# Optimization experiments

Measured on AMD Instinct MI355X. Metric: run time of the kernel, lower is better.

Reference implementation:

```python
import jax, jax.numpy as jnp
import numpy as np

N, E, H, DE = 50000, 800000, 128, 16

def silu(x):
    return x * jax.nn.sigmoid(x)

def setup_inputs() -> dict:
    key = jax.random.key(0)
    ks = jax.random.split(key, 24)
    def W(k, i, o, s=0.02):
        return (jax.random.normal(k, (i, o), jnp.float32) * s)
    inp = {
        'h': jax.random.normal(ks[0], (N, H), jnp.float32),
        'coord': jax.random.normal(ks[1], (N, 3), jnp.float32),
        'edge_index': jax.random.randint(ks[2], (2, E), 0, N),
        'edge_attr': jax.random.normal(ks[3], (E, DE), jnp.float32),
        # mes_mlp: Linear(2H+1+DE -> H), SiLU, Linear(H -> H), SiLU
        'mes_w1': W(ks[4], 2 * H + 1 + DE, H), 'mes_b1': jnp.zeros((H,), jnp.float32),
        'mes_w2': W(ks[5], H, H),              'mes_b2': jnp.zeros((H,), jnp.float32),
        # edge_mlp: Linear(H+1+DE -> H), SiLU, Linear(H -> H)
        'edge_w1': W(ks[6], H + 1 + DE, H),    'edge_b1': jnp.zeros((H,), jnp.float32),
        'edge_w2': W(ks[7], H, H),             'edge_b2': jnp.zeros((H,), jnp.float32),
        # node_mlp: Linear(H+H -> H), SiLU, Linear(H -> H)
        'node_w1': W(ks[8], 2 * H, H),         'node_b1': jnp.zeros((H,), jnp.float32),
        'node_w2': W(ks[9], H, H),             'node_b2': jnp.zeros((H,), jnp.float32),
        # coord_mlp: Linear(H -> H), SiLU, Linear(H -> 1, no bias, xavier gain 0.001)
        'coord_w1': W(ks[10], H, H),           'coord_b1': jnp.zeros((H,), jnp.float32),
        'coord_w2': W(ks[11], H, 1, s=0.001),
    }
    return inp

def reference(h, coord, edge_index, edge_attr,
              mes_w1, mes_b1, mes_w2, mes_b2,
              edge_w1, edge_b1, edge_w2, edge_b2,
              node_w1, node_b1, node_w2, node_b2,
              coord_w1, coord_b1, coord_w2):
    row, col = edge_index[0], edge_index[1]
    n = h.shape[0]
    # coord2radial
    coord_diff = coord[row] - coord[col]                        # [E,3]
    radial = jnp.sum(coord_diff ** 2, axis=1, keepdims=True)    # [E,1]
    norm = jnp.sqrt(radial + 1e-8)
    coord_diff = coord_diff / (norm + 1.0)
    # mes_model
    mes_in = jnp.concatenate([h[row], h[col], radial, edge_attr], axis=1)
    edge_feat = silu(silu(mes_in @ mes_w1 + mes_b1) @ mes_w2 + mes_b2)  # [E,H]
    # coord_model (agg='sum', no tanh)
    trans = coord_diff * (silu(edge_feat @ coord_w1 + coord_b1) @ coord_w2)  # [E,3]
    coord = coord + jax.ops.segment_sum(trans, col, num_segments=n)
    # node_model (recurrent)
    agg = jax.ops.segment_sum(edge_feat, col, num_segments=n)   # [N,H]
    node_in = jnp.concatenate([h, agg], axis=1)
    h = h + (silu(node_in @ node_w1 + node_b1) @ node_w2 + node_b2)
    # edge_model
    edge_in = jnp.concatenate([edge_feat, radial, edge_attr], axis=1)
    edge_out = silu(edge_in @ edge_w1 + edge_b1) @ edge_w2 + edge_b2
    return (h, coord, edge_out)
```

## Files before the change

kernel.cpp:

```cpp
#include <hip/hip_runtime.h>
#include <cstdint>
#include <cstddef>

typedef float f32x4 __attribute__((ext_vector_type(4)));
typedef __bf16 bf16x8 __attribute__((ext_vector_type(8)));
typedef unsigned short u16;

#define Hdim 128
#define DEdim 16
#define APITCH 296
#define FPITCH 168
#define NPITCH 264

__device__ __forceinline__ u16 f2bf(float f){
  uint32_t u = __builtin_bit_cast(uint32_t, f);
  u += 0x7fffu + ((u >> 16) & 1u);
  return (u16)(u >> 16);
}
__device__ __forceinline__ float silu_f(float x){
  return x / (1.0f + __expf(-x));
}

template<int KC>
__device__ __forceinline__ void gemm_tile(
    const u16* A, int apitch,
    const u16* __restrict__ Bt, int kpad,
    const float* __restrict__ bias,
    int wv, int cidx, int hi, f32x4 (&acc)[4][2])
{
  const int c0 = (wv*2+0)*16 + cidx;
  const int c1 = (wv*2+1)*16 + cidx;
  const float b0 = bias[c0];
  const float b1 = bias[c1];
  #pragma unroll
  for (int rt=0; rt<4; ++rt){
    acc[rt][0] = (f32x4){b0,b0,b0,b0};
    acc[rt][1] = (f32x4){b1,b1,b1,b1};
  }
  #pragma unroll
  for (int kc=0; kc<KC; ++kc){
    const int ko = kc*32 + hi*8;
    bf16x8 bb0 = *(const bf16x8*)(Bt + (size_t)c0*kpad + ko);
    bf16x8 bb1 = *(const bf16x8*)(Bt + (size_t)c1*kpad + ko);
    #pragma unroll
    for (int rt=0; rt<4; ++rt){
      bf16x8 a = *(const bf16x8*)(A + (rt*16+cidx)*apitch + ko);
      acc[rt][0] = __builtin_amdgcn_mfma_f32_16x16x32_bf16(a, bb0, acc[rt][0], 0,0,0);
      acc[rt][1] = __builtin_amdgcn_mfma_f32_16x16x32_bf16(a, bb1, acc[rt][1], 0,0,0);
    }
  }
}

__global__ __launch_bounds__(256, 2) void egcl_edge(
    const float* __restrict__ h, const float* __restrict__ coord,
    const int* __restrict__ ei, const float* __restrict__ ea,
    const float* __restrict__ mes_b1, const float* __restrict__ mes_b2,
    const float* __restrict__ edge_b1, const float* __restrict__ edge_b2,
    const float* __restrict__ coord_b1, const float* __restrict__ coord_w2,
    const u16* __restrict__ w_mes1t, const u16* __restrict__ w_mes2t,
    const u16* __restrict__ w_coord1t, const u16* __restrict__ w_edge1t,
    const u16* __restrict__ w_edge2t,
    float* __restrict__ agg, float* __restrict__ out_coord,
    float* __restrict__ out_edge, int E, int N)
{
  __shared__ u16 Ab[64*APITCH];
  __shared__ u16 Fb[64*FPITCH];
  __shared__ float cds[64*4];
  __shared__ float tvs[64];
  __shared__ int cnode[64];

  const int tid  = threadIdx.x;
  const int lane = tid & 63;
  const int wv   = tid >> 6;
  const int e0   = blockIdx.x * 64;
  const int cidx = lane & 15;
  const int hi   = lane >> 4;

  {
    const int le   = wv*16 + (lane>>2);
    const int part = lane & 3;
    int eg = e0 + le;
    if (eg >= E) eg = E-1;
    const int node = (part < 2) ? ei[eg] : ei[E + eg];
    const float* src = h + (size_t)node*Hdim + (part&1)*64;
    u16* dst = Ab + le*APITCH + part*64;
    #pragma unroll
    for (int j=0;j<16;++j){
      const float4 v = ((const float4*)src)[j];
      ushort4 o; o.x=f2bf(v.x); o.y=f2bf(v.y); o.z=f2bf(v.z); o.w=f2bf(v.w);
      *(ushort4*)(dst + j*4) = o;
    }
    if (part == 0){
      const int cn = ei[E + eg];
      const float dx = coord[(size_t)node*3+0] - coord[(size_t)cn*3+0];
      const float dy = coord[(size_t)node*3+1] - coord[(size_t)cn*3+1];
      const float dz = coord[(size_t)node*3+2] - coord[(size_t)cn*3+2];
      const float radial = dx*dx + dy*dy + dz*dz;
      const float inv = 1.0f/(sqrtf(radial + 1e-8f) + 1.0f);
      cds[le*4+0]=dx*inv; cds[le*4+1]=dy*inv; cds[le*4+2]=dz*inv; cds[le*4+3]=radial;
      cnode[le] = cn;
      const u16 rb = f2bf(radial);
      Ab[le*APITCH + 256] = rb;
      Fb[le*FPITCH + 128] = rb;
      #pragma unroll
      for (int j=0;j<DEdim;++j){
        const u16 v = f2bf(ea[(size_t)eg*DEdim + j]);
        Ab[le*APITCH + 257 + j] = v;
        Fb[le*FPITCH + 129 + j] = v;
      }
      #pragma unroll
      for (int j=273;j<288;++j) Ab[le*APITCH + j] = 0;
      #pragma unroll
      for (int j=145;j<160;++j) Fb[le*FPITCH + j] = 0;
    }
    if (tid < 64) tvs[tid] = 0.f;
  }
  __syncthreads();

  f32x4 acc[4][2];

  gemm_tile<9>(Ab, APITCH, w_mes1t, 288, mes_b1, wv, cidx, hi, acc);
  __syncthreads();
  #pragma unroll
  for (int rt=0; rt<4; ++rt)
    #pragma unroll
    for (int j=0;j<2;++j){
      const int col = (wv*2+j)*16 + cidx;
      #pragma unroll
      for (int i=0;i<4;++i)
        Ab[(rt*16 + hi*4 + i)*APITCH + col] = f2bf(silu_f(acc[rt][j][i]));
    }
  __syncthreads();

  gemm_tile<4>(Ab, APITCH, w_mes2t, 128, mes_b2, wv, cidx, hi, acc);
  #pragma unroll
  for (int rt=0; rt<4; ++rt)
    #pragma unroll
    for (int j=0;j<2;++j){
      const int col = (wv*2+j)*16 + cidx;
      #pragma unroll
      for (int i=0;i<4;++i){
        const int row = rt*16 + hi*4 + i;
        const float v = silu_f(acc[rt][j][i]);
        if (e0 + row < E)
          atomicAdd(agg + (size_t)cnode[row]*Hdim + col, v);
        Fb[row*FPITCH + col] = f2bf(v);
      }
    }
  __syncthreads();

  gemm_tile<4>(Fb, FPITCH, w_coord1t, 128, coord_b1, wv, cidx, hi, acc);
  {
    const float cw0 = coord_w2[(wv*2+0)*16 + cidx];
    const float cw1 = coord_w2[(wv*2+1)*16 + cidx];
    #pragma unroll
    for (int rt=0; rt<4; ++rt)
      #pragma unroll
      for (int i=0;i<4;++i){
        float p = silu_f(acc[rt][0][i])*cw0 + silu_f(acc[rt][1][i])*cw1;
        p += __shfl_xor(p, 1);
        p += __shfl_xor(p, 2);
        p += __shfl_xor(p, 4);
        p += __shfl_xor(p, 8);
        if (cidx == 0) atomicAdd(&tvs[rt*16 + hi*4 + i], p);
      }
  }
  __syncthreads();
  if (tid < 192){
    const int le = tid/3, d = tid%3;
    if (e0 + le < E)
      atomicAdd(out_coord + (size_t)cnode[le]*3 + d, cds[le*4+d]*tvs[le]);
  }

  gemm_tile<5>(Fb, FPITCH, w_edge1t, 160, edge_b1, wv, cidx, hi, acc);
  #pragma unroll
  for (int rt=0; rt<4; ++rt)
    #pragma unroll
    for (int j=0;j<2;++j){
      const int col = (wv*2+j)*16 + cidx;
      #pragma unroll
      for (int i=0;i<4;++i)
        Ab[(rt*16 + hi*4 + i)*APITCH + col] = f2bf(silu_f(acc[rt][j][i]));
    }
  __syncthreads();

  gemm_tile<4>(Ab, APITCH, w_edge2t, 128, edge_b2, wv, cidx, hi, acc);
  #pragma unroll
  for (int rt=0; rt<4; ++rt)
    #pragma unroll
    for (int j=0;j<2;++j){
      const int col = (wv*2+j)*16 + cidx;
      #pragma unroll
      for (int i=0;i<4;++i){
        const int row = rt*16 + hi*4 + i;
        const int eg = e0 + row;
        if (eg < E) out_edge[(size_t)eg*Hdim + col] = acc[rt][j][i];
      }
    }
}

__global__ __launch_bounds__(256, 2) void egcl_node(
    const float* __restrict__ h, const float* __restrict__ agg,
    const float* __restrict__ node_b1, const float* __restrict__ node_b2,
    const u16* __restrict__ w_node1t, const u16* __restrict__ w_node2t,
    float* __restrict__ out_h, int N)
{
  __shared__ u16 Ab[64*NPITCH];
  const int tid  = threadIdx.x;
  const int lane = tid & 63;
  const int wv   = tid >> 6;
  const int r0   = blockIdx.x * 64;
  const int cidx = lane & 15;
  const int hi   = lane >> 4;

  {
    const int le   = wv*16 + (lane>>2);
    const int part = lane & 3;
    int g = r0 + le;
    if (g >= N) g = N-1;
    const float* src = (part < 2) ? h   + (size_t)g*Hdim + part*64
                                  : agg + (size_t)g*Hdim + (part-2)*64;
    u16* dst = Ab + le*NPITCH + part*64;
    #pragma unroll
    for (int j=0;j<16;++j){
      const float4 v = ((const float4*)src)[j];
      ushort4 o; o.x=f2bf(v.x); o.y=f2bf(v.y); o.z=f2bf(v.z); o.w=f2bf(v.w);
      *(ushort4*)(dst + j*4) = o;
    }
  }
  __syncthreads();

  f32x4 acc[4][2];
  gemm_tile<8>(Ab, NPITCH, w_node1t, 256, node_b1, wv, cidx, hi, acc);
  __syncthreads();
  #pragma unroll
  for (int rt=0; rt<4; ++rt)
    #pragma unroll
    for (int j=0;j<2;++j){
      const int col = (wv*2+j)*16 + cidx;
      #pragma unroll
      for (int i=0;i<4;++i)
        Ab[(rt*16 + hi*4 + i)*NPITCH + col] = f2bf(silu_f(acc[rt][j][i]));
    }
  __syncthreads();
  gemm_tile<4>(Ab, NPITCH, w_node2t, 128, node_b2, wv, cidx, hi, acc);
  #pragma unroll
  for (int rt=0; rt<4; ++rt)
    #pragma unroll
    for (int j=0;j<2;++j){
      const int col = (wv*2+j)*16 + cidx;
      #pragma unroll
      for (int i=0;i<4;++i){
        const int row = rt*16 + hi*4 + i;
        const int g = r0 + row;
        if (g < N)
          out_h[(size_t)g*Hdim + col] = h[(size_t)g*Hdim + col] + acc[rt][j][i];
      }
    }
}

__global__ void egcl_init(float* __restrict__ agg, const float* __restrict__ coord,
                          float* __restrict__ out_coord, int nagg, int nc)
{
  const int i = blockIdx.x*256 + threadIdx.x;
  if (i < nagg) agg[i] = 0.f;
  if (i < nc)   out_coord[i] = coord[i];
}

__global__ void egcl_wconv(const float* __restrict__ src, u16* __restrict__ dst,
                           int K, int Kpad)
{
  const int i = blockIdx.x*256 + threadIdx.x;
  if (i >= 128*Kpad) return;
  const int c = i / Kpad, k = i - c*Kpad;
  const float v = (k < K) ? src[(size_t)k*128 + c] : 0.f;
  dst[i] = f2bf(v);
}

extern "C" void kernel_launch(void* const* d_in, const int* in_sizes, int n_in,
                              void* d_out, int out_size, void* d_ws, size_t ws_size,
                              hipStream_t stream)
{
  const float* h       = (const float*)d_in[0];
  const float* coord   = (const float*)d_in[1];
  const int*   ei      = (const int*)d_in[2];
  const float* ea      = (const float*)d_in[3];
  const float* mes_w1  = (const float*)d_in[4];
  const float* mes_b1  = (const float*)d_in[5];
  const float* mes_w2  = (const float*)d_in[6];
  const float* mes_b2  = (const float*)d_in[7];
  const float* edge_w1 = (const float*)d_in[8];
  const float* edge_b1 = (const float*)d_in[9];
  const float* edge_w2 = (const float*)d_in[10];
  const float* edge_b2 = (const float*)d_in[11];
  const float* node_w1 = (const float*)d_in[12];
  const float* node_b1 = (const float*)d_in[13];
  const float* node_w2 = (const float*)d_in[14];
  const float* node_b2 = (const float*)d_in[15];
  const float* coord_w1= (const float*)d_in[16];
  const float* coord_b1= (const float*)d_in[17];
  const float* coord_w2= (const float*)d_in[18];

  const int N = in_sizes[0] / Hdim;
  const int E = in_sizes[2] / 2;

  char* ws = (char*)d_ws;
  float* agg      = (float*)ws;
  u16* w_mes1t    = (u16*)(ws + (size_t)N*Hdim*4);
  u16* w_mes2t    = w_mes1t  + 128*288;
  u16* w_coord1t  = w_mes2t  + 128*128;
  u16* w_edge1t   = w_coord1t+ 128*128;
  u16* w_edge2t   = w_edge1t + 128*160;
  u16* w_node1t   = w_edge2t + 128*128;
  u16* w_node2t   = w_node1t + 128*256;

  float* out_h     = (float*)d_out;
  float* out_coord = out_h + (size_t)N*Hdim;
  float* out_edge  = out_coord + (size_t)N*3;

  egcl_init<<<(N*Hdim + 255)/256, 256, 0, stream>>>(agg, coord, out_coord, N*Hdim, N*3);

  egcl_wconv<<<(128*288 + 255)/256, 256, 0, stream>>>(mes_w1,   w_mes1t,   273, 288);
  egcl_wconv<<<(128*128 + 255)/256, 256, 0, stream>>>(mes_w2,   w_mes2t,   128, 128);
  egcl_wconv<<<(128*128 + 255)/256, 256, 0, stream>>>(coord_w1, w_coord1t, 128, 128);
  egcl_wconv<<<(128*160 + 255)/256, 256, 0, stream>>>(edge_w1,  w_edge1t,  145, 160);
  egcl_wconv<<<(128*128 + 255)/256, 256, 0, stream>>>(edge_w2,  w_edge2t,  128, 128);
  egcl_wconv<<<(128*256 + 255)/256, 256, 0, stream>>>(node_w1,  w_node1t,  256, 256);
  egcl_wconv<<<(128*128 + 255)/256, 256, 0, stream>>>(node_w2,  w_node2t,  128, 128);

  egcl_edge<<<(E + 63)/64, 256, 0, stream>>>(h, coord, ei, ea,
      mes_b1, mes_b2, edge_b1, edge_b2, coord_b1, coord_w2,
      w_mes1t, w_mes2t, w_coord1t, w_edge1t, w_edge2t,
      agg, out_coord, out_edge, E, N);

  egcl_node<<<(N + 63)/64, 256, 0, stream>>>(h, agg, node_b1, node_b2,
      w_node1t, w_node2t, out_h, N);
}
```

Baseline: 705.6 us.

## Replace edge-feature atomics with CSR gather aggregation in node kernel

Builds a CSR (histogram, scan, scatter) of incoming edges per node, stores the bf16 edge features to a workspace, and has the node kernel gather and sum them instead of doing E*H float atomicAdds into agg. It also drops the separate Fb LDS buffer by reusing a region of Ab, which cuts shared memory so launch bounds can move from 2 to 4 blocks per SM. This adds several small preprocessing kernels, a serial single-thread scan, extra global traffic for the feature buffer, and bf16 accumulation inputs. It falls back to the atomic path if the workspace is too small.

```diff
diff --git a/kernel.cpp b/kernel.cpp
--- a/kernel.cpp
+++ b/kernel.cpp
@@ -9,13 +9,19 @@
 #define Hdim 128
 #define DEdim 16
 #define APITCH 296
-#define FPITCH 168
+#define FOFF   136
 #define NPITCH 264
 
 __device__ __forceinline__ u16 f2bf(float f){
   uint32_t u = __builtin_bit_cast(uint32_t, f);
   u += 0x7fffu + ((u >> 16) & 1u);
   return (u16)(u >> 16);
+}
+__device__ __forceinline__ uint32_t pack_bf2(float a, float b){
+  return (uint32_t)f2bf(a) | ((uint32_t)f2bf(b) << 16);
+}
+__device__ __forceinline__ float bf2f(uint32_t lo16){
+  return __builtin_bit_cast(float, lo16 << 16);
 }
 __device__ __forceinline__ float silu_f(float x){
   return x / (1.0f + __expf(-x));
@@ -51,7 +57,8 @@
   }
 }
 
-__global__ __launch_bounds__(256, 2) void egcl_edge(
+template<bool GATHER>
+__global__ __launch_bounds__(256, 4) void egcl_edge(
     const float* __restrict__ h, const float* __restrict__ coord,
     const int* __restrict__ ei, const float* __restrict__ ea,
     const float* __restrict__ mes_b1, const float* __restrict__ mes_b2,
@@ -60,11 +67,10 @@
     const u16* __restrict__ w_mes1t, const u16* __restrict__ w_mes2t,
     const u16* __restrict__ w_coord1t, const u16* __restrict__ w_edge1t,
     const u16* __restrict__ w_edge2t,
-    float* __restrict__ agg, float* __restrict__ out_coord,
-    float* __restrict__ out_edge, int E, int N)
+    float* __restrict__ agg, u16* __restrict__ feat,
+    float* __restrict__ out_coord, float* __restrict__ out_edge, int E, int N)
 {
   __shared__ u16 Ab[64*APITCH];
-  __shared__ u16 Fb[64*FPITCH];
   __shared__ float cds[64*4];
   __shared__ float tvs[64];
   __shared__ int cnode[64];
@@ -99,19 +105,12 @@
       const float inv = 1.0f/(sqrtf(radial + 1e-8f) + 1.0f);
       cds[le*4+0]=dx*inv; cds[le*4+1]=dy*inv; cds[le*4+2]=dz*inv; cds[le*4+3]=radial;
       cnode[le] = cn;
-      const u16 rb = f2bf(radial);
-      Ab[le*APITCH + 256] = rb;
-      Fb[le*FPITCH + 128] = rb;
-      #pragma unroll
-      for (int j=0;j<DEdim;++j){
-        const u16 v = f2bf(ea[(size_t)eg*DEdim + j]);
-        Ab[le*APITCH + 257 + j] = v;
-        Fb[le*FPITCH + 129 + j] = v;
-      }
+      Ab[le*APITCH + 256] = f2bf(radial);
+      #pragma unroll
+      for (int j=0;j<DEdim;++j)
+        Ab[le*APITCH + 257 + j] = f2bf(ea[(size_t)eg*DEdim + j]);
       #pragma unroll
       for (int j=273;j<288;++j) Ab[le*APITCH + j] = 0;
-      #pragma unroll
-      for (int j=145;j<160;++j) Fb[le*FPITCH + j] = 0;
     }
     if (tid < 64) tvs[tid] = 0.f;
   }
@@ -130,6 +129,22 @@
       for (int i=0;i<4;++i)
         Ab[(rt*16 + hi*4 + i)*APITCH + col] = f2bf(silu_f(acc[rt][j][i]));
     }
+  if (tid < 64){
+    const int row = tid;
+    int eg = e0 + row; if (eg >= E) eg = E-1;
+    Ab[row*APITCH + FOFF + 128] = f2bf(cds[row*4+3]);
+    const float4* eap = (const float4*)(ea + (size_t)eg*DEdim);
+    #pragma unroll
+    for (int j=0;j<4;++j){
+      const float4 v = eap[j];
+      Ab[row*APITCH + FOFF + 129 + j*4 + 0] = f2bf(v.x);
+      Ab[row*APITCH + FOFF + 129 + j*4 + 1] = f2bf(v.y);
+      Ab[row*APITCH + FOFF + 129 + j*4 + 2] = f2bf(v.z);
+      Ab[row*APITCH + FOFF + 129 + j*4 + 3] = f2bf(v.w);
+    }
+    #pragma unroll
+    for (int j=145;j<160;++j) Ab[row*APITCH + FOFF + j] = 0;
+  }
   __syncthreads();
 
   gemm_tile<4>(Ab, APITCH, w_mes2t, 128, mes_b2, wv, cidx, hi, acc);
@@ -142,14 +157,23 @@
       for (int i=0;i<4;++i){
         const int row = rt*16 + hi*4 + i;
         const float v = silu_f(acc[rt][j][i]);
-        if (e0 + row < E)
+        if (!GATHER && e0 + row < E)
           atomicAdd(agg + (size_t)cnode[row]*Hdim + col, v);
-        Fb[row*FPITCH + col] = f2bf(v);
+        Ab[row*APITCH + FOFF + col] = f2bf(v);
       }
     }
   __syncthreads();
 
-  gemm_tile<4>(Fb, FPITCH, w_coord1t, 128, coord_b1, wv, cidx, hi, acc);
+  if (GATHER){
+    const int row = tid >> 2, seg = tid & 3;
+    if (e0 + row < E){
+      const int4* s = (const int4*)(Ab + row*APITCH + FOFF + seg*32);
+      int4* d = (int4*)(feat + (size_t)(e0+row)*Hdim + seg*32);
+      d[0]=s[0]; d[1]=s[1]; d[2]=s[2]; d[3]=s[3];
+    }
+  }
+
+  gemm_tile<4>(Ab + FOFF, APITCH, w_coord1t, 128, coord_b1, wv, cidx, hi, acc);
   {
     const float cw0 = coord_w2[(wv*2+0)*16 + cidx];
     const float cw1 = coord_w2[(wv*2+1)*16 + cidx];
@@ -172,7 +196,7 @@
       atomicAdd(out_coord + (size_t)cnode[le]*3 + d, cds[le*4+d]*tvs[le]);
   }
 
-  gemm_tile<5>(Fb, FPITCH, w_edge1t, 160, edge_b1, wv, cidx, hi, acc);
+  gemm_tile<5>(Ab + FOFF, APITCH, w_edge1t, 160, edge_b1, wv, cidx, hi, acc);
   #pragma unroll
   for (int rt=0; rt<4; ++rt)
     #pragma unroll
@@ -199,8 +223,11 @@
     }
 }
 
-__global__ __launch_bounds__(256, 2) void egcl_node(
+template<bool GATHER>
+__global__ __launch_bounds__(256, 4) void egcl_node(
     const float* __restrict__ h, const float* __restrict__ agg,
+    const int* __restrict__ offs, const int* __restrict__ deg,
+    const int* __restrict__ elist, const u16* __restrict__ feat,
     const float* __restrict__ node_b1, const float* __restrict__ node_b2,
     const u16* __restrict__ w_node1t, const u16* __restrict__ w_node2t,
     float* __restrict__ out_h, int N)
@@ -218,11 +245,55 @@
     const int part = lane & 3;
     int g = r0 + le;
     if (g >= N) g = N-1;
-    const float* src = (part < 2) ? h   + (size_t)g*Hdim + part*64
-                                  : agg + (size_t)g*Hdim + (part-2)*64;
-    u16* dst = Ab + le*NPITCH + part*64;
-    #pragma unroll
-    for (int j=0;j<16;++j){
+    const float* src = h + (size_t)g*Hdim + part*32;
+    u16* dst = Ab + le*NPITCH + part*32;
+    #pragma unroll
+    for (int j=0;j<8;++j){
+      const float4 v = ((const float4*)src)[j];
+      ushort4 o; o.x=f2bf(v.x); o.y=f2bf(v.y); o.z=f2bf(v.z); o.w=f2bf(v.w);
+      *(ushort4*)(dst + j*4) = o;
+    }
+  }
+  if (GATHER){
+    const uint32_t* fp = (const uint32_t*)feat;
+    for (int ln=0; ln<16; ++ln){
+      const int le = wv*16 + ln;
+      const int g = r0 + le;
+      float a0 = 0.f, a1 = 0.f;
+      if (g < N){
+        const int start = __builtin_amdgcn_readfirstlane(offs[g]);
+        const int dg    = __builtin_amdgcn_readfirstlane(deg[g]);
+        int d = 0;
+        for (; d + 4 <= dg; d += 4){
+          const int e0 = elist[start+d+0];
+          const int e1 = elist[start+d+1];
+          const int e2 = elist[start+d+2];
+          const int e3 = elist[start+d+3];
+          const uint32_t v0 = fp[(size_t)e0*64 + lane];
+          const uint32_t v1 = fp[(size_t)e1*64 + lane];
+          const uint32_t v2 = fp[(size_t)e2*64 + lane];
+          const uint32_t v3 = fp[(size_t)e3*64 + lane];
+          a0 += bf2f(v0 & 0xffffu) + bf2f(v1 & 0xffffu) + bf2f(v2 & 0xffffu) + bf2f(v3 & 0xffffu);
+          a1 += bf2f(v0 >> 16)     + bf2f(v1 >> 16)     + bf2f(v2 >> 16)     + bf2f(v3 >> 16);
+        }
+        for (; d < dg; ++d){
+          const int e = elist[start+d];
+          const uint32_t v = fp[(size_t)e*64 + lane];
+          a0 += bf2f(v & 0xffffu);
+          a1 += bf2f(v >> 16);
+        }
+      }
+      *(uint32_t*)&Ab[(size_t)le*NPITCH + 128 + lane*2] = pack_bf2(a0, a1);
+    }
+  } else {
+    const int le   = wv*16 + (lane>>2);
+    const int part = lane & 3;
+    int g = r0 + le;
+    if (g >= N) g = N-1;
+    const float* src = agg + (size_t)g*Hdim + part*32;
+    u16* dst = Ab + le*NPITCH + 128 + part*32;
+    #pragma unroll
+    for (int j=0;j<8;++j){
       const float4 v = ((const float4*)src)[j];
       ushort4 o; o.x=f2bf(v.x); o.y=f2bf(v.y); o.z=f2bf(v.z); o.w=f2bf(v.w);
       *(ushort4*)(dst + j*4) = o;
@@ -259,12 +330,14 @@
     }
 }
 
-__global__ void egcl_init(float* __restrict__ agg, const float* __restrict__ coord,
-                          float* __restrict__ out_coord, int nagg, int nc)
+__global__ void egcl_init(const float* __restrict__ coord, float* __restrict__ out_coord,
+                          int nc, float* __restrict__ zf, int nzf,
+                          int* __restrict__ zi, int nzi)
 {
   const int i = blockIdx.x*256 + threadIdx.x;
-  if (i < nagg) agg[i] = 0.f;
   if (i < nc)   out_coord[i] = coord[i];
+  if (zf && i < nzf) zf[i] = 0.f;
+  if (zi && i < nzi) zi[i] = 0;
 }
 
 __global__ void egcl_wconv(const float* __restrict__ src, u16* __restrict__ dst,
@@ -275,6 +348,50 @@
   const int c = i / Kpad, k = i - c*Kpad;
   const float v = (k < K) ? src[(size_t)k*128 + c] : 0.f;
   dst[i] = f2bf(v);
+}
+
+__global__ void k_hist(const int* __restrict__ ei, int* __restrict__ hist, int E){
+  const int i = blockIdx.x*256 + threadIdx.x;
+  if (i < E) atomicAdd(&hist[ei[E + i]], 1);
+}
+__global__ void k_scan1(const int* __restrict__ hist, int* __restrict__ partial, int N){
+  __shared__ int s[256];
+  const int t = threadIdx.x, i = blockIdx.x*256 + t;
+  s[t] = (i < N) ? hist[i] : 0;
+  __syncthreads();
+  for (int o=128; o>0; o>>=1){ if (t < o) s[t] += s[t+o]; __syncthreads(); }
+  if (t == 0) partial[blockIdx.x] = s[0];
+}
+__global__ void k_scan2(int* __restrict__ partial, int G){
+  if (blockIdx.x == 0 && threadIdx.x == 0){
+    int run = 0;
+    for (int i=0;i<G;++i){ const int v = partial[i]; partial[i] = run; run += v; }
+  }
+}
+__global__ void k_scan3(const int* __restrict__ hist, const int* __restrict__ partial,
+                        int* __restrict__ offs, int* __restrict__ cursor, int N){
+  __shared__ int s[256];
+  const int t = threadIdx.x, i = blockIdx.x*256 + t;
+  const int v = (i < N) ? hist[i] : 0;
+  s[t] = v;
+  __syncthreads();
+  for (int o=1; o<256; o<<=1){
+    int x = (t >= o) ? s[t-o] : 0;
+    __syncthreads();
+    s[t] += x;
+    __syncthreads();
+  }
+  const int ex = s[t] - v + partial[blockIdx.x];
+  if (i < N){ offs[i] = ex; cursor[i] = ex; }
+}
+__global__ void k_scatter(const int* __restrict__ ei, int* __restrict__ cursor,
+                          int* __restrict__ elist, int E){
+  const int i = blockIdx.x*256 + threadIdx.x;
+  if (i < E){
+    const int c = ei[E + i];
+    const int p = atomicAdd(&cursor[c], 1);
+    elist[p] = i;
+  }
 }
 
 extern "C" void kernel_launch(void* const* d_in, const int* in_sizes, int n_in,
@@ -303,36 +420,74 @@
 
   const int N = in_sizes[0] / Hdim;
   const int E = in_sizes[2] / 2;
+  const int G1 = (N + 255) / 256;
 
   char* ws = (char*)d_ws;
-  float* agg      = (float*)ws;
-  u16* w_mes1t    = (u16*)(ws + (size_t)N*Hdim*4);
+  u16* w_mes1t    = (u16*)ws;
   u16* w_mes2t    = w_mes1t  + 128*288;
   u16* w_coord1t  = w_mes2t  + 128*128;
   u16* w_edge1t   = w_coord1t+ 128*128;
   u16* w_edge2t   = w_edge1t + 128*160;
   u16* w_node1t   = w_edge2t + 128*128;
   u16* w_node2t   = w_node1t + 128*256;
+  const size_t woff = (((size_t)(288+128+128+160+128+256+128)*128*2) + 255) & ~(size_t)255;
+
+  auto align256 = [](size_t x){ return (x + 255) & ~(size_t)255; };
+  const size_t o_feat  = woff;
+  const size_t o_hist  = o_feat + align256((size_t)E*Hdim*2);
+  const size_t o_offs  = o_hist + align256((size_t)N*4);
+  const size_t o_cur   = o_offs + align256((size_t)N*4);
+  const size_t o_part  = o_cur  + align256((size_t)N*4);
+  const size_t o_elist = o_part + align256((size_t)G1*4);
+  const size_t need    = o_elist + (size_t)E*4;
+  const bool gather = (ws_size >= need);
 
   float* out_h     = (float*)d_out;
   float* out_coord = out_h + (size_t)N*Hdim;
   float* out_edge  = out_coord + (size_t)N*3;
 
-  egcl_init<<<(N*Hdim + 255)/256, 256, 0, stream>>>(agg, coord, out_coord, N*Hdim, N*3);
-
-  egcl_wconv<<<(128*288 + 255)/256, 256, 0, stream>>>(mes_w1,   w_mes1t,   273, 288);
+  egcl_wconv<<<(128*288 + 255)/256, 256, 0, stream>>>(mes_w1,   w_mes1t,   2*Hdim+1+DEdim, 288);
   egcl_wconv<<<(128*128 + 255)/256, 256, 0, stream>>>(mes_w2,   w_mes2t,   128, 128);
   egcl_wconv<<<(128*128 + 255)/256, 256, 0, stream>>>(coord_w1, w_coord1t, 128, 128);
-  egcl_wconv<<<(128*160 + 255)/256, 256, 0, stream>>>(edge_w1,  w_edge1t,  145, 160);
+  egcl_wconv<<<(128*160 + 255)/256, 256, 0, stream>>>(edge_w1,  w_edge1t,  Hdim+1+DEdim, 160);
   egcl_wconv<<<(128*128 + 255)/256, 256, 0, stream>>>(edge_w2,  w_edge2t,  128, 128);
   egcl_wconv<<<(128*256 + 255)/256, 256, 0, stream>>>(node_w1,  w_node1t,  256, 256);
   egcl_wconv<<<(128*128 + 255)/256, 256, 0, stream>>>(node_w2,  w_node2t,  128, 128);
 
-  egcl_edge<<<(E + 63)/64, 256, 0, stream>>>(h, coord, ei, ea,
-      mes_b1, mes_b2, edge_b1, edge_b2, coord_b1, coord_w2,
-      w_mes1t, w_mes2t, w_coord1t, w_edge1t, w_edge2t,
-      agg, out_coord, out_edge, E, N);
-
-  egcl_node<<<(N + 63)/64, 256, 0, stream>>>(h, agg, node_b1, node_b2,
-      w_node1t, w_node2t, out_h, N);
-}
+  if (gather){
+    u16* feat   = (u16*)(ws + o_feat);
+    int* hist   = (int*)(ws + o_hist);
+    int* offs   = (int*)(ws + o_offs);
+    int* cursor = (int*)(ws + o_cur);
+    int* partial= (int*)(ws + o_part);
+    int* elist  = (int*)(ws + o_elist);
+
+    egcl_init<<<(N*3 > N ? (N*3+255)/256 : (N+255)/256), 256, 0, stream>>>(
+        coord, out_coord, N*3, nullptr, 0, hist, N);
+    k_hist<<<(E + 255)/256, 256, 0, stream>>>(ei, hist, E);
+    k_scan1<<<G1, 256, 0, stream>>>(hist, partial, N);
+    k_scan2<<<1, 64, 0, stream>>>(partial, G1);
+    k_scan3<<<G1, 256, 0, stream>>>(hist, partial, offs, cursor, N);
+    k_scatter<<<(E + 255)/256, 256, 0, stream>>>(ei, cursor, elist, E);
+
+    egcl_edge<true><<<(E + 63)/64, 256, 0, stream>>>(h, coord, ei, ea,
+        mes_b1, mes_b2, edge_b1, edge_b2, coord_b1, coord_w2,
+        w_mes1t, w_mes2t, w_coord1t, w_edge1t, w_edge2t,
+        nullptr, feat, out_coord, out_edge, E, N);
+
+    egcl_node<true><<<(N + 63)/64, 256, 0, stream>>>(h, nullptr, offs, hist, elist, feat,
+        node_b1, node_b2, w_node1t, w_node2t, out_h, N);
+  } else {
+    float* agg = (float*)(ws + woff);
+    egcl_init<<<(N*Hdim + 255)/256, 256, 0, stream>>>(
+        coord, out_coord, N*3, agg, N*Hdim, nullptr, 0);
+
+    egcl_edge<false><<<(E + 63)/64, 256, 0, stream>>>(h, coord, ei, ea,
+        mes_b1, mes_b2, edge_b1, edge_b2, coord_b1, coord_w2,
+        w_mes1t, w_mes2t, w_coord1t, w_edge1t, w_edge2t,
+        agg, nullptr, out_coord, out_edge, E, N);
+
+    egcl_node<false><<<(N + 63)/64, 256, 0, stream>>>(h, agg, nullptr, nullptr, nullptr, nullptr,
+        node_b1, node_b2, w_node1t, w_node2t, out_h, N);
+  }
+}
```

Measured after the change: 718.2 us. Within noise of the previous version (+1.8%).
